# Performance work log

Hardware: AMD Instinct MI355X
Metric: run time of the kernel (lower is better)

## Reference

```python
import jax, jax.numpy as jnp
import numpy as np
from jax import lax

B, H_IMG, W_IMG = 512, 812, 40
HID = 128
NUM_CLASSES = 12
LSTM_IN = 32 * ((W_IMG - 5) // 2 + 1)  # 32 channels * 18 = 576


def setup_inputs() -> dict:
    key = jax.random.key(0)
    ks = jax.random.split(key, 20)
    s = 0.05
    inp = {
        "x": jax.random.normal(ks[0], (B, 1, H_IMG, W_IMG), jnp.float32),
        "conv_w": jax.random.normal(ks[1], (32, 1, 20, 5), jnp.float32) * s,
        "conv_b": jax.random.normal(ks[2], (32,), jnp.float32) * s,
        "Wih0": jax.random.normal(ks[3], (4 * HID, LSTM_IN), jnp.float32) * s,
        "Whh0": jax.random.normal(ks[4], (4 * HID, HID), jnp.float32) * s,
        "bih0": jax.random.normal(ks[5], (4 * HID,), jnp.float32) * s,
        "bhh0": jax.random.normal(ks[6], (4 * HID,), jnp.float32) * s,
        "Wih1": jax.random.normal(ks[7], (4 * HID, HID), jnp.float32) * s,
        "Whh1": jax.random.normal(ks[8], (4 * HID, HID), jnp.float32) * s,
        "bih1": jax.random.normal(ks[9], (4 * HID,), jnp.float32) * s,
        "bhh1": jax.random.normal(ks[10], (4 * HID,), jnp.float32) * s,
        "W_att": jax.random.normal(ks[11], (HID, HID), jnp.float32) * s,
        "b_att": jax.random.normal(ks[12], (HID,), jnp.float32) * s,
        "v_att": jax.random.normal(ks[13], (HID,), jnp.float32) * s,
        "W1": jax.random.normal(ks[14], (64, HID), jnp.float32) * s,
        "b1": jax.random.normal(ks[15], (64,), jnp.float32) * s,
        "W2": jax.random.normal(ks[16], (NUM_CLASSES, 64), jnp.float32) * s,
        "b2": jax.random.normal(ks[17], (NUM_CLASSES,), jnp.float32) * s,
    }
    return inp


def _lstm_layer(seq, Wih, Whh, bih, bhh):
    # seq: (T, B, I); PyTorch gate order i, f, g, o
    T, Bn, _ = seq.shape
    Hd = Whh.shape[1]
    x_proj = jnp.einsum('tbi,gi->tbg', seq, Wih) + bih + bhh  # (T,B,4H)

    def step(carry, xg):
        h, c = carry
        g = xg + h @ Whh.T
        i, f, gg, o = jnp.split(g, 4, axis=-1)
        c = jax.nn.sigmoid(f) * c + jax.nn.sigmoid(i) * jnp.tanh(gg)
        h = jax.nn.sigmoid(o) * jnp.tanh(c)
        return (h, c), h

    init = (jnp.zeros((Bn, Hd), seq.dtype), jnp.zeros((Bn, Hd), seq.dtype))
    _, hs = lax.scan(step, init, x_proj)
    return hs  # (T,B,H)


def _forward(x, conv_w, conv_b, Wih0, Whh0, bih0, bhh0, Wih1, Whh1, bih1, bhh1,
             W_att, b_att, v_att, W1, b1, W2, b2):
    # Conv2d(1->32, k=(20,5), s=(8,2)) + ReLU
    y = lax.conv_general_dilated(x, conv_w, (8, 2), 'VALID',
                                 dimension_numbers=('NCHW', 'OIHW', 'NCHW'))
    y = jax.nn.relu(y + conv_b[None, :, None, None])  # (B,32,T,W')
    b, c, t, w = y.shape
    # permute(0,2,3,1).view(b,t,-1).permute(1,0,2) -> (T,B,W'*32)
    seq = jnp.transpose(y, (2, 0, 3, 1)).reshape(t, b, w * c)
    # 2-layer LSTM (inter-layer dropout=0.2 inactive at eval)
    h1 = _lstm_layer(seq, Wih0, Whh0, bih0, bhh0)
    h2 = _lstm_layer(h1, Wih1, Whh1, bih1, bhh1)
    # additive attention pooling over time
    squish = jnp.tanh(jnp.einsum('tbh,hk->tbk', h2, W_att) + b_att)  # (T,B,H)
    attn = jnp.einsum('tbh,h->tb', squish, v_att)                     # (T,B)
    w_att_n = jax.nn.softmax(attn, axis=0)                            # softmax over T
    pooled = jnp.einsum('tb,tbh->bh', w_att_n, h2)                    # (B,H)
    # dnn1 -> (dropout inactive at eval) -> output
    hdn = pooled @ W1.T + b1
    return hdn @ W2.T + b2  # (B,num_classes)


def reference(x, conv_w, conv_b, Wih0, Whh0, bih0, bhh0, Wih1, Whh1, bih1, bhh1,
              W_att, b_att, v_att, W1, b1, W2, b2):
    return _forward(x, conv_w, conv_b, Wih0, Whh0, bih0, bhh0, Wih1, Whh1,
                    bih1, bhh1, W_att, b_att, v_att, W1, b1, W2, b2)
```

## Files before the change

### kernel.cpp

```cpp
#include <hip/hip_runtime.h>
#include <stdint.h>


#define T_STEPS 100
#define BATCH   512
#define HIDD    128
#define GATES   512
#define LSTMIN  576
#define HIMG    812
#define WIMG    40

typedef __attribute__((ext_vector_type(8))) short bf16x8;
typedef __attribute__((ext_vector_type(4))) float f32x4;
typedef __attribute__((ext_vector_type(2))) __fp16 f16x2;
typedef unsigned long long ull;

__device__ inline unsigned short f2bf(float f) {
  unsigned u = __float_as_uint(f);
  unsigned r = (u + 0x7fffu + ((u >> 16) & 1u)) >> 16;
  return (unsigned short)r;
}
__device__ inline unsigned pk_bf16(float a, float b) {
#if __has_builtin(__builtin_amdgcn_cvt_pk_bf16_f32)
  auto r = __builtin_amdgcn_cvt_pk_bf16_f32(a, b);
  return __builtin_bit_cast(unsigned, r);
#else
  return (unsigned)f2bf(a) | ((unsigned)f2bf(b) << 16);
#endif
}
__device__ inline float bf2f(unsigned short b) {
  return __uint_as_float(((unsigned)b) << 16);
}
__device__ inline float fsigm(float x) {
  float e = __expf(-x);
  return __builtin_amdgcn_rcpf(1.f + e);
}
__device__ inline float ftanh(float x) {
  float e = __expf(2.f * x);
  return (e - 1.f) * __builtin_amdgcn_rcpf(e + 1.f);
}
__device__ inline void lds_barrier() {
  asm volatile("s_waitcnt lgkmcnt(0)" ::: "memory");
  __builtin_amdgcn_s_barrier();
}
__device__ inline void wait_flag(int* fp, int need) {
  if ((threadIdx.x & 63) == 0) {
    while (__hip_atomic_load(fp, __ATOMIC_RELAXED, __HIP_MEMORY_SCOPE_AGENT) < need)
      __builtin_amdgcn_s_sleep(2);
  }
  asm volatile("" ::: "memory");
}

__global__ void prep_kernel(const float* __restrict__ Wih0, const float* __restrict__ Whh0,
                            const float* __restrict__ Wih1, const float* __restrict__ Whh1,
                            const float* __restrict__ Watt, const float* __restrict__ convw,
                            const float* __restrict__ bih0, const float* __restrict__ bhh0,
                            const float* __restrict__ bih1, const float* __restrict__ bhh1,
                            unsigned short* __restrict__ wih0b, unsigned short* __restrict__ whh0b,
                            unsigned short* __restrict__ wih1b, unsigned short* __restrict__ whh1b,
                            unsigned short* __restrict__ wattb, f16x2* __restrict__ wpair,
                            float* __restrict__ bias0, float* __restrict__ bias1,
                            int* __restrict__ flags) {
  int tid = blockIdx.x * blockDim.x + threadIdx.x;
  int stride = gridDim.x * blockDim.x;
  for (int i = tid; i < GATES * LSTMIN; i += stride) wih0b[i] = f2bf(Wih0[i]);
  for (int i = tid; i < GATES * HIDD; i += stride) whh0b[i] = f2bf(Whh0[i]);
  for (int i = tid; i < GATES * HIDD; i += stride) wih1b[i] = f2bf(Wih1[i]);
  for (int i = tid; i < GATES * HIDD; i += stride) whh1b[i] = f2bf(Whh1[i]);
  for (int i = tid; i < HIDD * HIDD; i += stride) {
    int j = i >> 7, k = i & 127;
    wattb[i] = f2bf(Watt[k * HIDD + j]);
  }
  for (int i = tid; i < 50 * 32; i += stride) {
    int k2 = i >> 5, c = i & 31;
    int kh2 = k2 / 5, kw = k2 % 5;
    float lo = convw[c * 100 + (2 * kh2) * 5 + kw];
    float hi = convw[c * 100 + (2 * kh2 + 1) * 5 + kw];
    wpair[i] = __builtin_amdgcn_cvt_pkrtz(lo, hi);
  }
  for (int i = tid; i < GATES; i += stride) bias0[i] = bih0[i] + bhh0[i];
  for (int i = tid; i < GATES; i += stride) bias1[i] = bih1[i] + bhh1[i];
  for (int i = tid; i < 32; i += stride) flags[i] = 0;
}

__global__ __launch_bounds__(256) void conv_kernel(const float* __restrict__ x,
                                                   const f16x2* __restrict__ wpair,
                                                   const float* __restrict__ convb,
                                                   unsigned short* __restrict__ seq) {
  __shared__ f16x2 imgp[106 * WIMG];
  const int b = blockIdx.x;
  const int chunk = blockIdx.y;
  const int t0 = chunk * 25;
  const float* src = x + (size_t)b * (HIMG * WIMG) + (size_t)(8 * t0) * WIMG;
  for (int i = threadIdx.x; i < 106 * WIMG; i += 256) {
    int r2 = i / WIMG, c = i % WIMG;
    float lo = src[(2 * r2) * WIMG + c];
    float hi = src[(2 * r2 + 1) * WIMG + c];
    imgp[i] = __builtin_amdgcn_cvt_pkrtz(lo, hi);
  }
  __syncthreads();
  for (int p = threadIdx.x; p < 450; p += 256) {
    int tl = p / 18, wp = p % 18;
    int t = t0 + tl;
    float acc[32];
#pragma unroll
    for (int c = 0; c < 32; ++c) acc[c] = 0.f;
    const f16x2* ibase = imgp + (4 * tl) * WIMG + 2 * wp;
#pragma unroll 2
    for (int kh2 = 0; kh2 < 10; ++kh2) {
#pragma unroll
      for (int kw = 0; kw < 5; ++kw) {
        f16x2 iv = ibase[kh2 * WIMG + kw];
        const f16x2* wk = wpair + (kh2 * 5 + kw) * 32;
#pragma unroll
        for (int c = 0; c < 32; ++c)
          acc[c] = __builtin_amdgcn_fdot2(iv, wk[c], acc[c], false);
      }
    }
    unsigned short* o = seq + ((size_t)(t * BATCH + b)) * LSTMIN + wp * 32;
#pragma unroll
    for (int c = 0; c < 32; ++c) {
      float v = acc[c] + convb[c];
      o[c] = f2bf(v > 0.f ? v : 0.f);
    }
  }
}

template <int KDIM>
__global__ __launch_bounds__(256) void gemm_xp_kernel(const unsigned short* __restrict__ A,
                                                      const unsigned short* __restrict__ Bw,
                                                      const float* __restrict__ bias,
                                                      unsigned short* __restrict__ Xp) {
  __shared__ __align__(16) unsigned short As[128 * 32];
  __shared__ __align__(16) unsigned short Bs[128 * 32];
  const int tid = threadIdx.x;
  const int lane = tid & 63;
  const int w = tid >> 6;
  const int col16 = lane & 15;
  const int q = lane >> 4;
  const int n0 = blockIdx.x * 128;
  const int m0 = blockIdx.y * 128;
  const int wm = (w & 1) * 64;
  const int wn = (w >> 1) * 64;
  f32x4 acc[4][4] = {};
  const int r = tid >> 2;
  const int sw = ((tid & 3) ^ (r & 3)) * 8;
  const unsigned wslot = (unsigned)w * 512;
  const unsigned short* ga = A + (size_t)(m0 + r) * KDIM + sw;
  const unsigned short* gb = Bw + (size_t)(n0 + r) * KDIM + sw;
  for (int k0 = 0; k0 < KDIM; k0 += 32) {
    __syncthreads();
    __builtin_amdgcn_global_load_lds((const __attribute__((address_space(1))) void*)(ga + k0),
                                     (__attribute__((address_space(3))) void*)(As + wslot), 16, 0, 0);
    __builtin_amdgcn_global_load_lds((const __attribute__((address_space(1))) void*)(ga + k0 + (size_t)64 * KDIM),
                                     (__attribute__((address_space(3))) void*)(As + wslot + 2048), 16, 0, 0);
    __builtin_amdgcn_global_load_lds((const __attribute__((address_space(1))) void*)(gb + k0),
                                     (__attribute__((address_space(3))) void*)(Bs + wslot), 16, 0, 0);
    __builtin_amdgcn_global_load_lds((const __attribute__((address_space(1))) void*)(gb + k0 + (size_t)64 * KDIM),
                                     (__attribute__((address_space(3))) void*)(Bs + wslot + 2048), 16, 0, 0);
    __syncthreads();
    bf16x8 af[4], bv[4];
#pragma unroll
    for (int i = 0; i < 4; ++i) {
      int ra = wm + i * 16 + col16;
      af[i] = *(const bf16x8*)(As + ra * 32 + ((q ^ (ra & 3)) * 8));
      int rb2 = wn + i * 16 + col16;
      bv[i] = *(const bf16x8*)(Bs + rb2 * 32 + ((q ^ (rb2 & 3)) * 8));
    }
#pragma unroll
    for (int i = 0; i < 4; ++i)
#pragma unroll
      for (int j = 0; j < 4; ++j)
        acc[i][j] = __builtin_amdgcn_mfma_f32_16x16x32_bf16(af[i], bv[j], acc[i][j], 0, 0, 0);
  }
#pragma unroll
  for (int ct = 0; ct < 4; ++ct) {
    int n = n0 + wn + ct * 16 + col16;
    float bvv = bias[n];
    int g = n >> 7;
    int rr2 = n & 127;
    int wqS = rr2 >> 5;
    int ntS = g * 2 + ((rr2 >> 4) & 1);
    int c16S = n & 15;
#pragma unroll
    for (int rt = 0; rt < 4; ++rt) {
      int m = m0 + wm + rt * 16 + q * 4;
      int t = m >> 9;
      int bb = m & 511;
      int blkS = bb >> 4;
      int r16 = bb & 15;
      ushort4 u;
      u.x = f2bf(acc[rt][ct][0] + bvv);
      u.y = f2bf(acc[rt][ct][1] + bvv);
      u.z = f2bf(acc[rt][ct][2] + bvv);
      u.w = f2bf(acc[rt][ct][3] + bvv);
      size_t tile = (((size_t)t * 32 + blkS) * 4 + wqS) * 8 + ntS;
      *(ushort4*)(Xp + tile * 256 + c16S * 16 + r16) = u;
    }
  }
}

__global__ __launch_bounds__(512, 2) void scan_pipe_kernel(
    const unsigned short* __restrict__ Xp0, const unsigned short* __restrict__ Whh0,
    const unsigned short* __restrict__ Wih1, const float* __restrict__ bias1,
    unsigned short* __restrict__ Xp1, const unsigned short* __restrict__ Whh1,
    unsigned short* __restrict__ hout, int* __restrict__ flags) {
  __shared__ __align__(16) unsigned short hb[2][16 * 136];
  const int tid = threadIdx.x;
  const int lane = tid & 63;
  const int w = tid >> 6;
  const int wq = w & 3;
  const int role = w >> 2;
  const int col16 = lane & 15;
  const int q = lane >> 4;
  const bool producer = blockIdx.x < 32;
  const int blk = producer ? (int)blockIdx.x : (int)blockIdx.x - 32;
  const int rb = blk * 16;
  int* flagp = flags + blk;
  const size_t TSTRIDE = (size_t)GATES * BATCH;
  const size_t TSTRIDE8 = TSTRIDE / 4;

  {
    unsigned short* hz = (unsigned short*)hb;
    for (int i = tid; i < 2 * 16 * 136; i += 512) hz[i] = 0;
  }

  if (producer) {
    if (role == 0) {
      bf16x8 bfrag[8][4];
      const unsigned short* xpb[8];
#pragma unroll
      for (int nt = 0; nt < 8; ++nt) {
        int cn = (nt >> 1) * HIDD + wq * 32 + (nt & 1) * 16 + col16;
#pragma unroll
        for (int ks = 0; ks < 4; ++ks)
          bfrag[nt][ks] = *(const bf16x8*)(Whh0 + (size_t)cn * HIDD + ks * 32 + q * 8);
        size_t tile = (((size_t)blk) * 4 + wq) * 8 + nt;
        xpb[nt] = Xp0 + tile * 256 + col16 * 16 + q * 4;
      }
      uint2 xb[2][8];
#pragma unroll
      for (int nt = 0; nt < 8; ++nt) xb[0][nt] = *(const uint2*)(xpb[nt]);
#pragma unroll
      for (int nt = 0; nt < 8; ++nt) xb[1][nt] = *(const uint2*)(xpb[nt] + TSTRIDE);
      float cst[8] = {0.f, 0.f, 0.f, 0.f, 0.f, 0.f, 0.f, 0.f};
      lds_barrier();
#pragma unroll 2
      for (int t = 0; t < T_STEPS; ++t) {
        const int s = t & 1;
        uint2 xv[8];
#pragma unroll
        for (int nt = 0; nt < 8; ++nt) xv[nt] = xb[s][nt];
        if (t + 2 < T_STEPS) {
#pragma unroll
          for (int nt = 0; nt < 8; ++nt)
            xb[s][nt] = *(const uint2*)(xpb[nt] + (size_t)(t + 2) * TSTRIDE);
        }
        bf16x8 af[4];
#pragma unroll
        for (int ks = 0; ks < 4; ++ks)
          af[ks] = *(const bf16x8*)(hb[s ^ 1] + col16 * 136 + ks * 32 + q * 8);
        f32x4 acc[8];
#pragma unroll
        for (int nt = 0; nt < 8; ++nt) {
          acc[nt][0] = __uint_as_float(xv[nt].x << 16);
          acc[nt][1] = __uint_as_float(xv[nt].x & 0xffff0000u);
          acc[nt][2] = __uint_as_float(xv[nt].y << 16);
          acc[nt][3] = __uint_as_float(xv[nt].y & 0xffff0000u);
        }
#pragma unroll
        for (int ks = 0; ks < 4; ++ks)
#pragma unroll
          for (int nt = 0; nt < 8; ++nt)
            acc[nt] = __builtin_amdgcn_mfma_f32_16x16x32_bf16(af[ks], bfrag[nt][ks], acc[nt], 0, 0, 0);
#pragma unroll
        for (int hh = 0; hh < 2; ++hh)
#pragma unroll
          for (int rr = 0; rr < 4; ++rr) {
            int idx = hh * 4 + rr;
            float pi = acc[0 + hh][rr];
            float pf = acc[2 + hh][rr];
            float pg = acc[4 + hh][rr];
            float po = acc[6 + hh][rr];
            float cc = fsigm(pf) * cst[idx] + fsigm(pi) * ftanh(pg);
            cst[idx] = cc;
            hb[s][(q * 4 + rr) * 136 + wq * 32 + hh * 16 + col16] = f2bf(fsigm(po) * ftanh(cc));
          }
        lds_barrier();
      }
      lds_barrier();
    } else {
      bf16x8 bfrag2[8][4];
      float biasn[8];
      ull* xob[8];
#pragma unroll
      for (int nt = 0; nt < 8; ++nt) {
        int cn = (nt >> 1) * HIDD + wq * 32 + (nt & 1) * 16 + col16;
#pragma unroll
        for (int ks = 0; ks < 4; ++ks)
          bfrag2[nt][ks] = *(const bf16x8*)(Wih1 + (size_t)cn * HIDD + ks * 32 + q * 8);
        biasn[nt] = bias1[cn];
        size_t tile = (((size_t)blk) * 4 + wq) * 8 + nt;
        xob[nt] = (ull*)(Xp1 + tile * 256 + col16 * 16 + q * 4);
      }
      lds_barrier();
#pragma unroll 2
      for (int t = 0; t < T_STEPS; ++t) {
        const int s = t & 1;
        if (t > 0) {
          bf16x8 af[4];
#pragma unroll
          for (int ks = 0; ks < 4; ++ks)
            af[ks] = *(const bf16x8*)(hb[s ^ 1] + col16 * 136 + ks * 32 + q * 8);
          f32x4 acc2[8];
#pragma unroll
          for (int nt = 0; nt < 8; ++nt) acc2[nt] = f32x4{0.f, 0.f, 0.f, 0.f};
#pragma unroll
          for (int ks = 0; ks < 4; ++ks)
#pragma unroll
            for (int nt = 0; nt < 8; ++nt)
              acc2[nt] = __builtin_amdgcn_mfma_f32_16x16x32_bf16(af[ks], bfrag2[nt][ks], acc2[nt], 0, 0, 0);
#pragma unroll
          for (int nt = 0; nt < 8; ++nt) {
            unsigned lo = pk_bf16(acc2[nt][0] + biasn[nt], acc2[nt][1] + biasn[nt]);
            unsigned hi = pk_bf16(acc2[nt][2] + biasn[nt], acc2[nt][3] + biasn[nt]);
            __hip_atomic_store(xob[nt] + (size_t)(t - 1) * TSTRIDE8,
                               (ull)lo | ((ull)hi << 32),
                               __ATOMIC_RELAXED, __HIP_MEMORY_SCOPE_AGENT);
          }
        }
        if ((t & 3) == 3) {
          asm volatile("s_waitcnt vmcnt(0) lgkmcnt(0)\ns_barrier" ::: "memory");
          if (tid == 256)
            __hip_atomic_store(flagp, t, __ATOMIC_RELAXED, __HIP_MEMORY_SCOPE_AGENT);
        } else {
          lds_barrier();
        }
      }
      {
        bf16x8 af[4];
#pragma unroll
        for (int ks = 0; ks < 4; ++ks)
          af[ks] = *(const bf16x8*)(hb[(T_STEPS - 1) & 1] + col16 * 136 + ks * 32 + q * 8);
        f32x4 acc2[8];
#pragma unroll
        for (int nt = 0; nt < 8; ++nt) acc2[nt] = f32x4{0.f, 0.f, 0.f, 0.f};
#pragma unroll
        for (int ks = 0; ks < 4; ++ks)
#pragma unroll
          for (int nt = 0; nt < 8; ++nt)
            acc2[nt] = __builtin_amdgcn_mfma_f32_16x16x32_bf16(af[ks], bfrag2[nt][ks], acc2[nt], 0, 0, 0);
#pragma unroll
        for (int nt = 0; nt < 8; ++nt) {
          unsigned lo = pk_bf16(acc2[nt][0] + biasn[nt], acc2[nt][1] + biasn[nt]);
          unsigned hi = pk_bf16(acc2[nt][2] + biasn[nt], acc2[nt][3] + biasn[nt]);
          __hip_atomic_store(xob[nt] + (size_t)(T_STEPS - 1) * TSTRIDE8,
                             (ull)lo | ((ull)hi << 32),
                             __ATOMIC_RELAXED, __HIP_MEMORY_SCOPE_AGENT);
        }
        asm volatile("s_waitcnt vmcnt(0) lgkmcnt(0)\ns_barrier" ::: "memory");
        if (tid == 256)
          __hip_atomic_store(flagp, 100, __ATOMIC_RELAXED, __HIP_MEMORY_SCOPE_AGENT);
      }
    }
  } else {
    if (role == 0) {
      bf16x8 bfrag[8][4];
      ull* xpb[8];
#pragma unroll
      for (int nt = 0; nt < 8; ++nt) {
        int cn = (nt >> 1) * HIDD + wq * 32 + (nt & 1) * 16 + col16;
#pragma unroll
        for (int ks = 0; ks < 4; ++ks)
          bfrag[nt][ks] = *(const bf16x8*)(Whh1 + (size_t)cn * HIDD + ks * 32 + q * 8);
        size_t tile = (((size_t)blk) * 4 + wq) * 8 + nt;
        xpb[nt] = (ull*)(Xp1 + tile * 256 + col16 * 16 + q * 4);
      }
      wait_flag(flagp, 6);
      ull xb[2][8];
#pragma unroll
      for (int nt = 0; nt < 8; ++nt)
        xb[0][nt] = __hip_atomic_load(xpb[nt], __ATOMIC_RELAXED, __HIP_MEMORY_SCOPE_AGENT);
#pragma unroll
      for (int nt = 0; nt < 8; ++nt)
        xb[1][nt] = __hip_atomic_load(xpb[nt] + TSTRIDE8, __ATOMIC_RELAXED, __HIP_MEMORY_SCOPE_AGENT);
      float cst[8] = {0.f, 0.f, 0.f, 0.f, 0.f, 0.f, 0.f, 0.f};
      lds_barrier();
#pragma unroll 2
      for (int t = 0; t < T_STEPS; ++t) {
        if (t > 0 && (t & 3) == 0) {
          int need = t + 6;
          if (need > 100) need = 100;
          wait_flag(flagp, need);
        }
        const int s = t & 1;
        ull xv[8];
#pragma unroll
        for (int nt = 0; nt < 8; ++nt) xv[nt] = xb[s][nt];
        if (t + 2 < T_STEPS) {
#pragma unroll
          for (int nt = 0; nt < 8; ++nt)
            xb[s][nt] = __hip_atomic_load(xpb[nt] + (size_t)(t + 2) * TSTRIDE8,
                                          __ATOMIC_RELAXED, __HIP_MEMORY_SCOPE_AGENT);
        }
        bf16x8 af[4];
#pragma unroll
        for (int ks = 0; ks < 4; ++ks)
          af[ks] = *(const bf16x8*)(hb[s ^ 1] + col16 * 136 + ks * 32 + q * 8);
        f32x4 acc[8];
#pragma unroll
        for (int nt = 0; nt < 8; ++nt) {
          unsigned lo = (unsigned)xv[nt];
          unsigned hi = (unsigned)(xv[nt] >> 32);
          acc[nt][0] = __uint_as_float(lo << 16);
          acc[nt][1] = __uint_as_float(lo & 0xffff0000u);
          acc[nt][2] = __uint_as_float(hi << 16);
          acc[nt][3] = __uint_as_float(hi & 0xffff0000u);
        }
#pragma unroll
        for (int ks = 0; ks < 4; ++ks)
#pragma unroll
          for (int nt = 0; nt < 8; ++nt)
            acc[nt] = __builtin_amdgcn_mfma_f32_16x16x32_bf16(af[ks], bfrag[nt][ks], acc[nt], 0, 0, 0);
#pragma unroll
        for (int hh = 0; hh < 2; ++hh)
#pragma unroll
          for (int rr = 0; rr < 4; ++rr) {
            int idx = hh * 4 + rr;
            float pi = acc[0 + hh][rr];
            float pf = acc[2 + hh][rr];
            float pg = acc[4 + hh][rr];
            float po = acc[6 + hh][rr];
            float cc = fsigm(pf) * cst[idx] + fsigm(pi) * ftanh(pg);
            cst[idx] = cc;
            hb[s][(q * 4 + rr) * 136 + wq * 32 + hh * 16 + col16] = f2bf(fsigm(po) * ftanh(cc));
          }
        lds_barrier();
      }
    } else {
      const int c = wq * 64 + lane;
      const int row = c >> 4;
      const int ch = c & 15;
      lds_barrier();
#pragma unroll 2
      for (int t = 0; t < T_STEPS; ++t) {
        if (t > 0) {
          uint4 hx = *(const uint4*)(hb[(t - 1) & 1] + row * 136 + ch * 8);
          *(uint4*)(hout + ((size_t)((t - 1) * BATCH) + rb + row) * HIDD + ch * 8) = hx;
        }
        lds_barrier();
      }
      uint4 hx = *(const uint4*)(hb[(T_STEPS - 1) & 1] + row * 136 + ch * 8);
      *(uint4*)(hout + ((size_t)((T_STEPS - 1) * BATCH) + rb + row) * HIDD + ch * 8) = hx;
    }
  }
}

__global__ __launch_bounds__(256) void gemm_att_kernel(const unsigned short* __restrict__ A,
                                                       const unsigned short* __restrict__ Bw,
                                                       const float* __restrict__ b_att,
                                                       const float* __restrict__ v_att,
                                                       float* __restrict__ scores) {
  __shared__ __align__(16) unsigned short As[128 * 32];
  __shared__ __align__(16) unsigned short Bs[128 * 32];
  __shared__ float s_red[128];
  const int tid = threadIdx.x;
  const int lane = tid & 63;
  const int w = tid >> 6;
  const int col16 = lane & 15;
  const int q = lane >> 4;
  const int m0 = blockIdx.y * 128;
  const int wm = (w & 1) * 64;
  const int wn = (w >> 1) * 64;
  f32x4 acc[4][4] = {};
  const int r = tid >> 2;
  const int sw = ((tid & 3) ^ (r & 3)) * 8;
  const unsigned wslot = (unsigned)w * 512;
  const unsigned short* ga = A + (size_t)(m0 + r) * HIDD + sw;
  const unsigned short* gb = Bw + (size_t)r * HIDD + sw;
  for (int k0 = 0; k0 < HIDD; k0 += 32) {
    __syncthreads();
    __builtin_amdgcn_global_load_lds((const __attribute__((address_space(1))) void*)(ga + k0),
                                     (__attribute__((address_space(3))) void*)(As + wslot), 16, 0, 0);
    __builtin_amdgcn_global_load_lds((const __attribute__((address_space(1))) void*)(ga + k0 + (size_t)64 * HIDD),
                                     (__attribute__((address_space(3))) void*)(As + wslot + 2048), 16, 0, 0);
    __builtin_amdgcn_global_load_lds((const __attribute__((address_space(1))) void*)(gb + k0),
                                     (__attribute__((address_space(3))) void*)(Bs + wslot), 16, 0, 0);
    __builtin_amdgcn_global_load_lds((const __attribute__((address_space(1))) void*)(gb + k0 + (size_t)64 * HIDD),
                                     (__attribute__((address_space(3))) void*)(Bs + wslot + 2048), 16, 0, 0);
    __syncthreads();
    bf16x8 af[4], bv[4];
#pragma unroll
    for (int i = 0; i < 4; ++i) {
      int ra = wm + i * 16 + col16;
      af[i] = *(const bf16x8*)(As + ra * 32 + ((q ^ (ra & 3)) * 8));
      int rb2 = wn + i * 16 + col16;
      bv[i] = *(const bf16x8*)(Bs + rb2 * 32 + ((q ^ (rb2 & 3)) * 8));
    }
#pragma unroll
    for (int i = 0; i < 4; ++i)
#pragma unroll
      for (int j = 0; j < 4; ++j)
        acc[i][j] = __builtin_amdgcn_mfma_f32_16x16x32_bf16(af[i], bv[j], acc[i][j], 0, 0, 0);
  }
  if (tid < 128) s_red[tid] = 0.f;
  float rs[4][4];
#pragma unroll
  for (int rt = 0; rt < 4; ++rt)
#pragma unroll
    for (int rr = 0; rr < 4; ++rr) rs[rt][rr] = 0.f;
#pragma unroll
  for (int ct = 0; ct < 4; ++ct) {
    int n = wn + ct * 16 + col16;
    float bvv = b_att[n], vv = v_att[n];
#pragma unroll
    for (int rt = 0; rt < 4; ++rt)
#pragma unroll
      for (int rr = 0; rr < 4; ++rr) {
        float xv2 = acc[rt][ct][rr] + bvv;
        float e = __expf(2.f * xv2);
        rs[rt][rr] += vv * (e - 1.f) * __builtin_amdgcn_rcpf(e + 1.f);
      }
  }
#pragma unroll
  for (int off = 1; off < 16; off <<= 1)
#pragma unroll
    for (int rt = 0; rt < 4; ++rt)
#pragma unroll
      for (int rr = 0; rr < 4; ++rr) rs[rt][rr] += __shfl_xor(rs[rt][rr], off, 64);
  __syncthreads();
  if (col16 == 0) {
#pragma unroll
    for (int rt = 0; rt < 4; ++rt)
#pragma unroll
      for (int rr = 0; rr < 4; ++rr)
        atomicAdd(&s_red[wm + rt * 16 + q * 4 + rr], rs[rt][rr]);
  }
  __syncthreads();
  if (tid < 128) scores[m0 + tid] = s_red[tid];
}

__global__ __launch_bounds__(128) void final_kernel(const float* __restrict__ scores,
                                                    const unsigned short* __restrict__ h2,
                                                    const float* __restrict__ W1, const float* __restrict__ b1,
                                                    const float* __restrict__ W2, const float* __restrict__ b2,
                                                    float* __restrict__ out) {
  const int b = blockIdx.x;
  const int tid = threadIdx.x;
  __shared__ float wj[T_STEPS];
  __shared__ float red[128];
  __shared__ float pooled[128];
  __shared__ float hdn[64];
  float sv = (tid < T_STEPS) ? scores[tid * BATCH + b] : -1e30f;
  red[tid] = sv;
  __syncthreads();
#pragma unroll
  for (int off = 64; off > 0; off >>= 1) {
    if (tid < off) red[tid] = fmaxf(red[tid], red[tid + off]);
    __syncthreads();
  }
  float mx = red[0];
  __syncthreads();
  float ev = (tid < T_STEPS) ? __expf(sv - mx) : 0.f;
  red[tid] = ev;
  __syncthreads();
#pragma unroll
  for (int off = 64; off > 0; off >>= 1) {
    if (tid < off) red[tid] += red[tid + off];
    __syncthreads();
  }
  float inv = 1.0f / red[0];
  if (tid < T_STEPS) wj[tid] = ev * inv;
  __syncthreads();
  float p = 0.f;
#pragma unroll 4
  for (int t = 0; t < T_STEPS; ++t)
    p += wj[t] * bf2f(h2[((size_t)(t * BATCH + b)) * HIDD + tid]);
  pooled[tid] = p;
  __syncthreads();
  if (tid < 64) {
    float a = b1[tid];
    for (int h = 0; h < 128; ++h) a = fmaf(W1[tid * 128 + h], pooled[h], a);
    hdn[tid] = a;
  }
  __syncthreads();
  if (tid < 12) {
    float a = b2[tid];
    for (int j = 0; j < 64; ++j) a = fmaf(W2[tid * 64 + j], hdn[j], a);
    out[b * 12 + tid] = a;
  }
}

extern "C" void kernel_launch(void* const* d_in, const int* in_sizes, int n_in,
                              void* d_out, int out_size, void* d_ws, size_t ws_size,
                              hipStream_t stream) {
  (void)in_sizes; (void)n_in; (void)out_size; (void)ws_size;
  const float* x      = (const float*)d_in[0];
  const float* conv_w = (const float*)d_in[1];
  const float* conv_b = (const float*)d_in[2];
  const float* Wih0   = (const float*)d_in[3];
  const float* Whh0   = (const float*)d_in[4];
  const float* bih0   = (const float*)d_in[5];
  const float* bhh0   = (const float*)d_in[6];
  const float* Wih1   = (const float*)d_in[7];
  const float* Whh1   = (const float*)d_in[8];
  const float* bih1   = (const float*)d_in[9];
  const float* bhh1   = (const float*)d_in[10];
  const float* W_att  = (const float*)d_in[11];
  const float* b_att  = (const float*)d_in[12];
  const float* v_att  = (const float*)d_in[13];
  const float* W1     = (const float*)d_in[14];
  const float* b1     = (const float*)d_in[15];
  const float* W2     = (const float*)d_in[16];
  const float* b2     = (const float*)d_in[17];

  char* ws = (char*)d_ws;
  size_t off = 0;
  auto carve = [&](size_t bytes) { char* p = ws + off; off += (bytes + 255) & ~(size_t)255; return p; };
  unsigned short* seq    = (unsigned short*)carve((size_t)T_STEPS * BATCH * LSTMIN * 2);
  unsigned short* xp0    = (unsigned short*)carve((size_t)T_STEPS * GATES * BATCH * 2);
  unsigned short* h2     = (unsigned short*)carve((size_t)T_STEPS * BATCH * HIDD * 2);
  float*          scores = (float*)carve((size_t)T_STEPS * BATCH * 4);
  unsigned short* wih0b  = (unsigned short*)carve((size_t)GATES * LSTMIN * 2);
  unsigned short* whh0b  = (unsigned short*)carve((size_t)GATES * HIDD * 2);
  unsigned short* wih1b  = (unsigned short*)carve((size_t)GATES * HIDD * 2);
  unsigned short* whh1b  = (unsigned short*)carve((size_t)GATES * HIDD * 2);
  unsigned short* wattb  = (unsigned short*)carve((size_t)HIDD * HIDD * 2);
  f16x2*          wpair  = (f16x2*)carve(50 * 32 * 4);
  float*          bias0  = (float*)carve(GATES * 4);
  float*          bias1  = (float*)carve(GATES * 4);
  int*            flags  = (int*)carve(32 * 4);
  unsigned short* xp1 = seq;

  prep_kernel<<<256, 256, 0, stream>>>(Wih0, Whh0, Wih1, Whh1, W_att, conv_w,
                                       bih0, bhh0, bih1, bhh1,
                                       wih0b, whh0b, wih1b, whh1b, wattb, wpair,
                                       bias0, bias1, flags);
  conv_kernel<<<dim3(512, 4), 256, 0, stream>>>(x, wpair, conv_b, seq);
  gemm_xp_kernel<LSTMIN><<<dim3(4, 400), 256, 0, stream>>>(seq, wih0b, bias0, xp0);
  scan_pipe_kernel<<<64, 512, 0, stream>>>(xp0, whh0b, wih1b, bias1, xp1, whh1b, h2, flags);
  gemm_att_kernel<<<dim3(1, 400), 256, 0, stream>>>(h2, wattb, b_att, v_att, scores);
  final_kernel<<<512, 128, 0, stream>>>(scores, h2, W1, b1, W2, b2, (float*)d_out);
}
```

Baseline: 421.1 us.

## Share weight tile across two M halves in input GEMM and restructure attention GEMM

The input-projection GEMM now launches 512-thread blocks that cover two 128-row M tiles, with the Wih0 tile loaded into LDS once and shared, which halves weight traffic per output. The attention GEMM is rewritten so each block loads all of W_att into LDS once, keeps h2 fragments in registers, and computes a 256-row score tile. This removes the K loop and the LDS atomics, and uses ftanh in place of the explicit exp-based tanh. The scan kernel only gains local aliases for the LDS double buffers.

After: 424.0 us. About the same (+0.7%).

```diff
diff --git a/kernel.cpp b/kernel.cpp
--- a/kernel.cpp
+++ b/kernel.cpp
@@ -126,38 +126,46 @@
   }
 }
 
-template <int KDIM>
-__global__ __launch_bounds__(256) void gemm_xp_kernel(const unsigned short* __restrict__ A,
+__global__ __launch_bounds__(512) void gemm576_kernel(const unsigned short* __restrict__ seq,
                                                       const unsigned short* __restrict__ Bw,
                                                       const float* __restrict__ bias,
                                                       unsigned short* __restrict__ Xp) {
-  __shared__ __align__(16) unsigned short As[128 * 32];
-  __shared__ __align__(16) unsigned short Bs[128 * 32];
+  __shared__ __align__(16) unsigned short As_s[2][4096];
+  __shared__ __align__(16) unsigned short Bs_s[4096];
   const int tid = threadIdx.x;
-  const int lane = tid & 63;
-  const int w = tid >> 6;
+  const int g = blockIdx.x;
+  const int mp = g >> 2;
+  const int nb = g & 3;
+  const int half = tid >> 8;
+  const int t256 = tid & 255;
+  const int m0 = mp * 256 + half * 128;
+  const int n0 = nb * 128;
+  const int tt = mp >> 1;
+  unsigned short* As = As_s[half];
+  const int lane = t256 & 63;
+  const int w4 = t256 >> 6;
   const int col16 = lane & 15;
   const int q = lane >> 4;
-  const int n0 = blockIdx.x * 128;
-  const int m0 = blockIdx.y * 128;
-  const int wm = (w & 1) * 64;
-  const int wn = (w >> 1) * 64;
+  const int wm = (w4 & 1) * 64;
+  const int wn = (w4 >> 1) * 64;
   f32x4 acc[4][4] = {};
-  const int r = tid >> 2;
-  const int sw = ((tid & 3) ^ (r & 3)) * 8;
-  const unsigned wslot = (unsigned)w * 512;
-  const unsigned short* ga = A + (size_t)(m0 + r) * KDIM + sw;
-  const unsigned short* gb = Bw + (size_t)(n0 + r) * KDIM + sw;
-  for (int k0 = 0; k0 < KDIM; k0 += 32) {
+  const int r = t256 >> 2;
+  const int sw = ((t256 & 3) ^ (r & 3)) * 8;
+  const unsigned wslot = (unsigned)w4 * 512;
+  const unsigned short* ga = seq + (size_t)(m0 + r) * LSTMIN + sw;
+  const unsigned short* gb = Bw + (size_t)(n0 + r) * LSTMIN + sw;
+  for (int k0 = 0; k0 < LSTMIN; k0 += 32) {
     __syncthreads();
     __builtin_amdgcn_global_load_lds((const __attribute__((address_space(1))) void*)(ga + k0),
                                      (__attribute__((address_space(3))) void*)(As + wslot), 16, 0, 0);
-    __builtin_amdgcn_global_load_lds((const __attribute__((address_space(1))) void*)(ga + k0 + (size_t)64 * KDIM),
+    __builtin_amdgcn_global_load_lds((const __attribute__((address_space(1))) void*)(ga + k0 + (size_t)64 * LSTMIN),
                                      (__attribute__((address_space(3))) void*)(As + wslot + 2048), 16, 0, 0);
-    __builtin_amdgcn_global_load_lds((const __attribute__((address_space(1))) void*)(gb + k0),
-                                     (__attribute__((address_space(3))) void*)(Bs + wslot), 16, 0, 0);
-    __builtin_amdgcn_global_load_lds((const __attribute__((address_space(1))) void*)(gb + k0 + (size_t)64 * KDIM),
-                                     (__attribute__((address_space(3))) void*)(Bs + wslot + 2048), 16, 0, 0);
+    if (half == 0) {
+      __builtin_amdgcn_global_load_lds((const __attribute__((address_space(1))) void*)(gb + k0),
+                                       (__attribute__((address_space(3))) void*)(Bs_s + wslot), 16, 0, 0);
+      __builtin_amdgcn_global_load_lds((const __attribute__((address_space(1))) void*)(gb + k0 + (size_t)64 * LSTMIN),
+                                       (__attribute__((address_space(3))) void*)(Bs_s + wslot + 2048), 16, 0, 0);
+    }
     __syncthreads();
     bf16x8 af[4], bv[4];
 #pragma unroll
@@ -165,7 +173,7 @@
       int ra = wm + i * 16 + col16;
       af[i] = *(const bf16x8*)(As + ra * 32 + ((q ^ (ra & 3)) * 8));
       int rb2 = wn + i * 16 + col16;
-      bv[i] = *(const bf16x8*)(Bs + rb2 * 32 + ((q ^ (rb2 & 3)) * 8));
+      bv[i] = *(const bf16x8*)(Bs_s + rb2 * 32 + ((q ^ (rb2 & 3)) * 8));
     }
 #pragma unroll
     for (int i = 0; i < 4; ++i)
@@ -177,24 +185,19 @@
   for (int ct = 0; ct < 4; ++ct) {
     int n = n0 + wn + ct * 16 + col16;
     float bvv = bias[n];
-    int g = n >> 7;
-    int rr2 = n & 127;
-    int wqS = rr2 >> 5;
-    int ntS = g * 2 + ((rr2 >> 4) & 1);
-    int c16S = n & 15;
+    int g2 = n >> 7, rr2 = n & 127;
+    int wqS = rr2 >> 5, ntS = g2 * 2 + ((rr2 >> 4) & 1), c16S = n & 15;
 #pragma unroll
     for (int rt = 0; rt < 4; ++rt) {
       int m = m0 + wm + rt * 16 + q * 4;
-      int t = m >> 9;
       int bb = m & 511;
-      int blkS = bb >> 4;
-      int r16 = bb & 15;
+      int blkS = bb >> 4, r16 = bb & 15;
       ushort4 u;
       u.x = f2bf(acc[rt][ct][0] + bvv);
       u.y = f2bf(acc[rt][ct][1] + bvv);
       u.z = f2bf(acc[rt][ct][2] + bvv);
       u.w = f2bf(acc[rt][ct][3] + bvv);
-      size_t tile = (((size_t)t * 32 + blkS) * 4 + wqS) * 8 + ntS;
+      size_t tile = (((size_t)tt * 32 + blkS) * 4 + wqS) * 8 + ntS;
       *(ushort4*)(Xp + tile * 256 + c16S * 16 + r16) = u;
     }
   }
@@ -248,6 +251,8 @@
 #pragma unroll 2
       for (int t = 0; t < T_STEPS; ++t) {
         const int s = t & 1;
+        unsigned short* hw = hb[s];
+        unsigned short* hr = hb[s ^ 1];
         uint2 xv[8];
 #pragma unroll
         for (int nt = 0; nt < 8; ++nt) xv[nt] = xb[s][nt];
@@ -259,7 +264,7 @@
         bf16x8 af[4];
 #pragma unroll
         for (int ks = 0; ks < 4; ++ks)
-          af[ks] = *(const bf16x8*)(hb[s ^ 1] + col16 * 136 + ks * 32 + q * 8);
+          af[ks] = *(const bf16x8*)(hr + col16 * 136 + ks * 32 + q * 8);
         f32x4 acc[8];
 #pragma unroll
         for (int nt = 0; nt < 8; ++nt) {
@@ -284,7 +289,7 @@
             float po = acc[6 + hh][rr];
             float cc = fsigm(pf) * cst[idx] + fsigm(pi) * ftanh(pg);
             cst[idx] = cc;
-            hb[s][(q * 4 + rr) * 136 + wq * 32 + hh * 16 + col16] = f2bf(fsigm(po) * ftanh(cc));
+            hw[(q * 4 + rr) * 136 + wq * 32 + hh * 16 + col16] = f2bf(fsigm(po) * ftanh(cc));
           }
         lds_barrier();
       }
@@ -307,11 +312,12 @@
 #pragma unroll 2
       for (int t = 0; t < T_STEPS; ++t) {
         const int s = t & 1;
+        unsigned short* hr = hb[s ^ 1];
         if (t > 0) {
           bf16x8 af[4];
 #pragma unroll
           for (int ks = 0; ks < 4; ++ks)
-            af[ks] = *(const bf16x8*)(hb[s ^ 1] + col16 * 136 + ks * 32 + q * 8);
+            af[ks] = *(const bf16x8*)(hr + col16 * 136 + ks * 32 + q * 8);
           f32x4 acc2[8];
 #pragma unroll
           for (int nt = 0; nt < 8; ++nt) acc2[nt] = f32x4{0.f, 0.f, 0.f, 0.f};
@@ -338,10 +344,11 @@
         }
       }
       {
+        unsigned short* hr = hb[(T_STEPS - 1) & 1];
         bf16x8 af[4];
 #pragma unroll
         for (int ks = 0; ks < 4; ++ks)
-          af[ks] = *(const bf16x8*)(hb[(T_STEPS - 1) & 1] + col16 * 136 + ks * 32 + q * 8);
+          af[ks] = *(const bf16x8*)(hr + col16 * 136 + ks * 32 + q * 8);
         f32x4 acc2[8];
 #pragma unroll
         for (int nt = 0; nt < 8; ++nt) acc2[nt] = f32x4{0.f, 0.f, 0.f, 0.f};
@@ -394,6 +401,8 @@
           wait_flag(flagp, need);
         }
         const int s = t & 1;
+        unsigned short* hw = hb[s];
+        unsigned short* hr = hb[s ^ 1];
         ull xv[8];
 #pragma unroll
         for (int nt = 0; nt < 8; ++nt) xv[nt] = xb[s][nt];
@@ -406,7 +415,7 @@
         bf16x8 af[4];
 #pragma unroll
         for (int ks = 0; ks < 4; ++ks)
-          af[ks] = *(const bf16x8*)(hb[s ^ 1] + col16 * 136 + ks * 32 + q * 8);
+          af[ks] = *(const bf16x8*)(hr + col16 * 136 + ks * 32 + q * 8);
         f32x4 acc[8];
 #pragma unroll
         for (int nt = 0; nt < 8; ++nt) {
@@ -433,7 +442,7 @@
             float po = acc[6 + hh][rr];
             float cc = fsigm(pf) * cst[idx] + fsigm(pi) * ftanh(pg);
             cst[idx] = cc;
-            hb[s][(q * 4 + rr) * 136 + wq * 32 + hh * 16 + col16] = f2bf(fsigm(po) * ftanh(cc));
+            hw[(q * 4 + rr) * 136 + wq * 32 + hh * 16 + col16] = f2bf(fsigm(po) * ftanh(cc));
           }
         lds_barrier();
       }
@@ -456,88 +465,75 @@
   }
 }
 
-__global__ __launch_bounds__(256) void gemm_att_kernel(const unsigned short* __restrict__ A,
-                                                       const unsigned short* __restrict__ Bw,
-                                                       const float* __restrict__ b_att,
-                                                       const float* __restrict__ v_att,
-                                                       float* __restrict__ scores) {
-  __shared__ __align__(16) unsigned short As[128 * 32];
-  __shared__ __align__(16) unsigned short Bs[128 * 32];
-  __shared__ float s_red[128];
+__global__ __launch_bounds__(256) void att_kernel(const unsigned short* __restrict__ A,
+                                                  const unsigned short* __restrict__ Bw,
+                                                  const float* __restrict__ b_att,
+                                                  const float* __restrict__ v_att,
+                                                  float* __restrict__ scores) {
+  __shared__ __align__(16) unsigned short Bs[4][4096];
+  __shared__ float s_red[256];
   const int tid = threadIdx.x;
   const int lane = tid & 63;
   const int w = tid >> 6;
   const int col16 = lane & 15;
   const int q = lane >> 4;
-  const int m0 = blockIdx.y * 128;
-  const int wm = (w & 1) * 64;
-  const int wn = (w >> 1) * 64;
-  f32x4 acc[4][4] = {};
-  const int r = tid >> 2;
-  const int sw = ((tid & 3) ^ (r & 3)) * 8;
-  const unsigned wslot = (unsigned)w * 512;
-  const unsigned short* ga = A + (size_t)(m0 + r) * HIDD + sw;
-  const unsigned short* gb = Bw + (size_t)r * HIDD + sw;
-  for (int k0 = 0; k0 < HIDD; k0 += 32) {
-    __syncthreads();
-    __builtin_amdgcn_global_load_lds((const __attribute__((address_space(1))) void*)(ga + k0),
-                                     (__attribute__((address_space(3))) void*)(As + wslot), 16, 0, 0);
-    __builtin_amdgcn_global_load_lds((const __attribute__((address_space(1))) void*)(ga + k0 + (size_t)64 * HIDD),
-                                     (__attribute__((address_space(3))) void*)(As + wslot + 2048), 16, 0, 0);
-    __builtin_amdgcn_global_load_lds((const __attribute__((address_space(1))) void*)(gb + k0),
-                                     (__attribute__((address_space(3))) void*)(Bs + wslot), 16, 0, 0);
-    __builtin_amdgcn_global_load_lds((const __attribute__((address_space(1))) void*)(gb + k0 + (size_t)64 * HIDD),
-                                     (__attribute__((address_space(3))) void*)(Bs + wslot + 2048), 16, 0, 0);
-    __syncthreads();
-    bf16x8 af[4], bv[4];
-#pragma unroll
-    for (int i = 0; i < 4; ++i) {
-      int ra = wm + i * 16 + col16;
-      af[i] = *(const bf16x8*)(As + ra * 32 + ((q ^ (ra & 3)) * 8));
-      int rb2 = wn + i * 16 + col16;
-      bv[i] = *(const bf16x8*)(Bs + rb2 * 32 + ((q ^ (rb2 & 3)) * 8));
-    }
+  const int m0 = blockIdx.x * 256;
+  for (int gi = tid; gi < 2048; gi += 256) {
+    int n = gi >> 4;
+    int ks = (gi >> 2) & 3;
+    int qg = gi & 3;
+    bf16x8 v = *(const bf16x8*)(Bw + n * 128 + ks * 32 + qg * 8);
+    *(bf16x8*)(Bs[ks] + n * 32 + ((qg ^ (n & 3)) * 8)) = v;
+  }
+  __syncthreads();
+  bf16x8 af[4][4];
+#pragma unroll
+  for (int i = 0; i < 4; ++i) {
+    const unsigned short* ar = A + (size_t)(m0 + w * 64 + i * 16 + col16) * HIDD;
+#pragma unroll
+    for (int ks = 0; ks < 4; ++ks)
+      af[i][ks] = *(const bf16x8*)(ar + ks * 32 + q * 8);
+  }
+  float rs[4][4];
+#pragma unroll
+  for (int i = 0; i < 4; ++i)
+#pragma unroll
+    for (int rr = 0; rr < 4; ++rr) rs[i][rr] = 0.f;
+#pragma unroll
+  for (int nt = 0; nt < 8; ++nt) {
+    int n = nt * 16 + col16;
+    bf16x8 bv[4];
+#pragma unroll
+    for (int ks = 0; ks < 4; ++ks)
+      bv[ks] = *(const bf16x8*)(Bs[ks] + n * 32 + ((q ^ (n & 3)) * 8));
+    f32x4 acc[4] = {};
+#pragma unroll
+    for (int ks = 0; ks < 4; ++ks)
+#pragma unroll
+      for (int i = 0; i < 4; ++i)
+        acc[i] = __builtin_amdgcn_mfma_f32_16x16x32_bf16(af[i][ks], bv[ks], acc[i], 0, 0, 0);
+    float bvv = b_att[n], vv = v_att[n];
 #pragma unroll
     for (int i = 0; i < 4; ++i)
 #pragma unroll
-      for (int j = 0; j < 4; ++j)
-        acc[i][j] = __builtin_amdgcn_mfma_f32_16x16x32_bf16(af[i], bv[j], acc[i][j], 0, 0, 0);
-  }
-  if (tid < 128) s_red[tid] = 0.f;
-  float rs[4][4];
-#pragma unroll
-  for (int rt = 0; rt < 4; ++rt)
-#pragma unroll
-    for (int rr = 0; rr < 4; ++rr) rs[rt][rr] = 0.f;
-#pragma unroll
-  for (int ct = 0; ct < 4; ++ct) {
-    int n = wn + ct * 16 + col16;
-    float bvv = b_att[n], vv = v_att[n];
-#pragma unroll
-    for (int rt = 0; rt < 4; ++rt)
-#pragma unroll
-      for (int rr = 0; rr < 4; ++rr) {
-        float xv2 = acc[rt][ct][rr] + bvv;
-        float e = __expf(2.f * xv2);
-        rs[rt][rr] += vv * (e - 1.f) * __builtin_amdgcn_rcpf(e + 1.f);
-      }
+      for (int rr = 0; rr < 4; ++rr)
+        rs[i][rr] += vv * ftanh(acc[i][rr] + bvv);
   }
 #pragma unroll
   for (int off = 1; off < 16; off <<= 1)
 #pragma unroll
-    for (int rt = 0; rt < 4; ++rt)
-#pragma unroll
-      for (int rr = 0; rr < 4; ++rr) rs[rt][rr] += __shfl_xor(rs[rt][rr], off, 64);
-  __syncthreads();
+    for (int i = 0; i < 4; ++i)
+#pragma unroll
+      for (int rr = 0; rr < 4; ++rr) rs[i][rr] += __shfl_xor(rs[i][rr], off, 64);
   if (col16 == 0) {
 #pragma unroll
-    for (int rt = 0; rt < 4; ++rt)
+    for (int i = 0; i < 4; ++i)
 #pragma unroll
       for (int rr = 0; rr < 4; ++rr)
-        atomicAdd(&s_red[wm + rt * 16 + q * 4 + rr], rs[rt][rr]);
-  }
-  __syncthreads();
-  if (tid < 128) scores[m0 + tid] = s_red[tid];
+        s_red[w * 64 + i * 16 + q * 4 + rr] = rs[i][rr];
+  }
+  __syncthreads();
+  scores[m0 + tid] = s_red[tid];
 }
 
 __global__ __launch_bounds__(128) void final_kernel(const float* __restrict__ scores,
@@ -637,8 +633,8 @@
                                        wih0b, whh0b, wih1b, whh1b, wattb, wpair,
                                        bias0, bias1, flags);
   conv_kernel<<<dim3(512, 4), 256, 0, stream>>>(x, wpair, conv_b, seq);
-  gemm_xp_kernel<LSTMIN><<<dim3(4, 400), 256, 0, stream>>>(seq, wih0b, bias0, xp0);
+  gemm576_kernel<<<800, 512, 0, stream>>>(seq, wih0b, bias0, xp0);
   scan_pipe_kernel<<<64, 512, 0, stream>>>(xp0, whh0b, wih1b, bias1, xp1, whh1b, h2, flags);
-  gemm_att_kernel<<<dim3(1, 400), 256, 0, stream>>>(h2, wattb, b_att, v_att, scores);
+  att_kernel<<<200, 256, 0, stream>>>(h2, wattb, b_att, v_att, scores);
   final_kernel<<<512, 128, 0, stream>>>(scores, h2, W1, b1, W2, b2, (float*)d_out);
 }
```
